# Kernel optimization log

Measured on AMD Instinct MI355X. Metric: run time of the kernel, lower is better.

Reference implementation:

```python
import jax, jax.numpy as jnp
import numpy as np

B, L = 8, 2048
AMP, ANG = 48, 16
H = 4
AQK, GQK = 12, 6   # amp/ang qk head dims
AV, GV = 12, 6     # amp/ang v head dims
LOOKBACK = 100


def setup_inputs() -> dict:
    key = jax.random.key(0)
    ks = jax.random.split(key, 16)
    def w(k, i, o):
        # kaiming-uniform-ish scale; stored [in, out] so forward is x @ W
        bound = 1.0 / np.sqrt(i)
        return jax.random.uniform(k, (i, o), jnp.float32, -bound, bound)
    return dict(
        x_ang=jax.random.normal(ks[0], (B, L, 2 * ANG), jnp.float32),
        x_amp=jax.random.normal(ks[1], (B, L, AMP), jnp.float32),
        Wq_amp=w(ks[2], AMP, H * AQK),
        Wk_amp=w(ks[3], AMP, H * AQK),
        Wv_amp=w(ks[4], AMP, H * AV),
        Wq_ang_r=w(ks[5], ANG, H * GQK),
        Wq_ang_i=w(ks[6], ANG, H * GQK),
        Wk_ang_r=w(ks[7], ANG, H * GQK),
        Wk_ang_i=w(ks[8], ANG, H * GQK),
        Wv_ang_r=w(ks[9], ANG, H * GV),
        Wv_ang_i=w(ks[10], ANG, H * GV),
        Wout_amp=w(ks[11], H * AV, AMP),
        bout_amp=jax.random.uniform(ks[12], (AMP,), jnp.float32, -0.1, 0.1),
        Wout_ang_r=w(ks[13], H * GV, ANG),
        Wout_ang_i=w(ks[14], H * GV, ANG),
    )


def _clin(xr, xi, Wr, Wi):
    # complex linear: (xr + i xi) @ (Wr + i Wi)
    return xr @ Wr - xi @ Wi, xr @ Wi + xi @ Wr


def reference(x_ang, x_amp, Wq_amp, Wk_amp, Wv_amp,
              Wq_ang_r, Wq_ang_i, Wk_ang_r, Wk_ang_i,
              Wv_ang_r, Wv_ang_i, Wout_amp, bout_amp,
              Wout_ang_r, Wout_ang_i):
    Bb, Ll, CA = x_ang.shape
    ang_r, ang_i = jnp.split(x_ang, 2, axis=-1)

    def heads(x, hd):  # [B,L,H*hd] -> [B,H,L,hd]
        return x.reshape(Bb, Ll, H, hd).transpose(0, 2, 1, 3)

    q_amp = heads(x_amp @ Wq_amp, AQK)
    k_amp = heads(x_amp @ Wk_amp, AQK)
    qar, qai = _clin(ang_r, ang_i, Wq_ang_r, Wq_ang_i)
    kar, kai = _clin(ang_r, ang_i, Wk_ang_r, Wk_ang_i)
    q = jnp.concatenate([heads(qar, GQK), heads(qai, GQK), q_amp], axis=-1)  # [B,H,L,24]
    k = jnp.concatenate([heads(kar, GQK), heads(kai, GQK), k_amp], axis=-1)

    v_amp = heads(x_amp @ Wv_amp, AV)
    var, vai = _clin(ang_r, ang_i, Wv_ang_r, Wv_ang_i)
    v = jnp.concatenate([heads(var, GV), heads(vai, GV), v_amp], axis=-1)  # [B,H,L,24]

    scale = 1.0 / jnp.sqrt(jnp.asarray(q.shape[-1], q.dtype))
    scores = jnp.einsum('bhqd,bhkd->bhqk', q, k) * scale
    idx = jnp.arange(Ll)
    valid = (idx[None, :] <= idx[:, None]) & (idx[None, :] >= idx[:, None] - (LOOKBACK - 1))
    mask = jnp.where(valid, jnp.asarray(0.0, scores.dtype), jnp.finfo(scores.dtype).min)
    attn = jax.nn.softmax(scores + mask, axis=-1)
    out = jnp.einsum('bhqk,bhkd->bhqd', attn, v)  # [B,H,L,24]

    o_ang_r, o_ang_i, o_amp = jnp.split(out, [GV, 2 * GV], axis=-1)

    def merge(x):  # [B,H,L,hd] -> [B,L,H*hd]
        return x.transpose(0, 2, 1, 3).reshape(Bb, Ll, -1)

    out_amp = merge(o_amp) @ Wout_amp + bout_amp
    out_ang_r, out_ang_i = _clin(merge(o_ang_r), merge(o_ang_i), Wout_ang_r, Wout_ang_i)
    return (out_ang_r, out_ang_i, out_amp)
```

## Files before the change

### kernel.cpp

```cpp
#include <hip/hip_runtime.h>
#include <hip/hip_bf16.h>
#include <hip/hip_fp16.h>

constexpr int B = 8;
constexpr int L = 2048;
constexpr int ANG = 16;
constexpr int AMP = 48;
constexpr int H = 4;
constexpr int AQK = 12, GQK = 6;
constexpr int AV = 12, GV = 6;
constexpr int HD = 2 * GQK + AQK;
constexpr int LOOKBACK = 100;
constexpr int NTOK = B * L;

typedef __fp16 f16x2 __attribute__((ext_vector_type(2)));

__device__ inline f16x2 pkrtz(float a, float b) {
    return __builtin_amdgcn_cvt_pkrtz(a, b);
}
__device__ inline float2 up2(f16x2 v) { return make_float2((float)v[0], (float)v[1]); }

union F4H { float4 v; f16x2 h[4]; };

constexpr int TQ     = 64;
constexpr int GROUPS = 4;
constexpr int CHUNK  = 25;
constexpr int MAXK   = TQ + LOOKBACK - 1;
constexpr int NT     = L / TQ;

struct StageT { f16x2 xall[MAXK][41]; };
struct TileT  {
    float4 Ks[MAXK][3];
    float4 Vs[MAXK][3];
    float4 Qs[TQ][7];
};
union SharedU { StageT s; TileT t; };

__device__ inline void proj_row(const f16x2* __restrict__ xrow, int h,
                                const float* __restrict__ Wamp,
                                const float* __restrict__ Wang_r,
                                const float* __restrict__ Wang_i,
                                float out[24])
{
    float a[12];
    #pragma unroll
    for (int c = 0; c < 12; ++c) a[c] = 0.f;
    #pragma unroll
    for (int i2 = 0; i2 < 24; ++i2) {
        float2 x2 = up2(xrow[i2]);
        const float* w0 = Wamp + (2 * i2) * 48 + h * AQK;
        const float* w1 = Wamp + (2 * i2 + 1) * 48 + h * AQK;
        #pragma unroll
        for (int c = 0; c < 12; ++c)
            a[c] += x2.x * w0[c] + x2.y * w1[c];
    }
    float rr[6], im[6];
    #pragma unroll
    for (int c = 0; c < 6; ++c) { rr[c] = 0.f; im[c] = 0.f; }
    #pragma unroll
    for (int i2 = 0; i2 < 8; ++i2) {
        float2 xr2 = up2(xrow[24 + i2]);
        float2 xi2 = up2(xrow[32 + i2]);
        const float* wr0 = Wang_r + (2 * i2) * 24 + h * GQK;
        const float* wi0 = Wang_i + (2 * i2) * 24 + h * GQK;
        const float* wr1 = Wang_r + (2 * i2 + 1) * 24 + h * GQK;
        const float* wi1 = Wang_i + (2 * i2 + 1) * 24 + h * GQK;
        #pragma unroll
        for (int c = 0; c < 6; ++c) {
            rr[c] += xr2.x * wr0[c] - xi2.x * wi0[c] + xr2.y * wr1[c] - xi2.y * wi1[c];
            im[c] += xr2.x * wi0[c] + xi2.x * wr0[c] + xr2.y * wi1[c] + xi2.y * wr1[c];
        }
    }
    #pragma unroll
    for (int c = 0; c < 6; ++c) { out[c] = rr[c]; out[6 + c] = im[c]; }
    #pragma unroll
    for (int c = 0; c < 12; ++c) out[12 + c] = a[c];
}

__global__ __launch_bounds__(256, 2) void fused_qkv_attn5_kernel(
    const float* __restrict__ x_ang, const float* __restrict__ x_amp,
    const float* __restrict__ Wq_amp, const float* __restrict__ Wk_amp,
    const float* __restrict__ Wv_amp,
    const float* __restrict__ Wq_ang_r, const float* __restrict__ Wq_ang_i,
    const float* __restrict__ Wk_ang_r, const float* __restrict__ Wk_ang_i,
    const float* __restrict__ Wv_ang_r, const float* __restrict__ Wv_ang_i,
    float* __restrict__ att)
{
    __shared__ SharedU u;

    const int tid = threadIdx.x;
    const int bh  = blockIdx.x / NT;
    const int qt  = blockIdx.x % NT;
    const int b   = bh / H, h = bh % H;
    const int q0  = qt * TQ;
    int kmin = q0 - (LOOKBACK - 1); if (kmin < 0) kmin = 0;
    const int nrows = q0 + TQ - kmin;
    const int qoff  = q0 - kmin;

    {
        const float4* xm4 = (const float4*)(x_amp + ((size_t)b * L + kmin) * AMP);
        const float4* xg4 = (const float4*)(x_ang + ((size_t)b * L + kmin) * (2 * ANG));
        int namp = nrows * 12;
        int ntot = namp + nrows * 8;
        for (int c = tid; c < ntot; c += 256) {
            if (c < namp) {
                int r = c / 12, i = c % 12;
                float4 t4 = xm4[c];
                u.s.xall[r][2 * i]     = pkrtz(t4.x, t4.y);
                u.s.xall[r][2 * i + 1] = pkrtz(t4.z, t4.w);
            } else {
                int c2 = c - namp;
                int r = c2 / 8, i = c2 % 8;
                float4 t4 = xg4[c2];
                u.s.xall[r][24 + 2 * i]     = pkrtz(t4.x, t4.y);
                u.s.xall[r][24 + 2 * i + 1] = pkrtz(t4.z, t4.w);
            }
        }
    }
    __syncthreads();

    const bool kvact = (tid < nrows);
    const bool qact  = (tid >= 192);
    const int  qrow  = tid - 192;

    float kd[24], vd[24], qd[24];
    if (kvact) {
        const f16x2* xrow = u.s.xall[tid];
        proj_row(xrow, h, Wk_amp, Wk_ang_r, Wk_ang_i, kd);
        proj_row(xrow, h, Wv_amp, Wv_ang_r, Wv_ang_i, vd);
    }
    if (qact) {
        const f16x2* xrow = u.s.xall[qoff + qrow];
        proj_row(xrow, h, Wq_amp, Wq_ang_r, Wq_ang_i, qd);
    }
    __syncthreads();

    if (kvact) {
        int r = tid;
        #pragma unroll
        for (int sl = 0; sl < 3; ++sl) {
            F4H pk_, pv_;
            #pragma unroll
            for (int j = 0; j < 4; ++j) {
                pk_.h[j] = pkrtz(kd[8 * sl + 2 * j], kd[8 * sl + 2 * j + 1]);
                pv_.h[j] = pkrtz(vd[8 * sl + 2 * j], vd[8 * sl + 2 * j + 1]);
            }
            u.t.Ks[r][sl] = pk_.v;
            u.t.Vs[r][sl] = pv_.v;
        }
    } else if (tid < MAXK) {
        float4 z = make_float4(0.f, 0.f, 0.f, 0.f);
        #pragma unroll
        for (int sl = 0; sl < 3; ++sl) { u.t.Ks[tid][sl] = z; u.t.Vs[tid][sl] = z; }
    }
    if (qact) {
        #pragma unroll
        for (int s = 0; s < 6; ++s)
            u.t.Qs[qrow][s] = make_float4(qd[4*s], qd[4*s+1], qd[4*s+2], qd[4*s+3]);
    }
    __syncthreads();

    const int lane = tid & 63;
    const int w    = tid >> 6;
    const int q16  = lane & 15;
    const int g    = lane >> 4;
    const int ql   = w * 16 + q16;
    const int qi   = q0 + ql;

    float qf[24];
    #pragma unroll
    for (int s = 0; s < 6; ++s) {
        float4 t4 = u.t.Qs[ql][s];
        qf[4*s] = t4.x; qf[4*s+1] = t4.y; qf[4*s+2] = t4.z; qf[4*s+3] = t4.w;
    }

    const float scale = 0.2041241452319315f;
    int j0 = qi - (LOOKBACK - 1); if (j0 < 0) j0 = 0;
    const int jstart = j0 + g;

    float sc[CHUNK];
    #pragma unroll
    for (int t = 0; t < CHUNK; ++t) {
        int j = jstart + t * GROUPS;
        int r = j - kmin;
        F4H k0, k1, k2;
        k0.v = u.t.Ks[r][0]; k1.v = u.t.Ks[r][1]; k2.v = u.t.Ks[r][2];
        float d = 0.f;
        #pragma unroll
        for (int jj = 0; jj < 4; ++jj) {
            float2 a0 = up2(k0.h[jj]); d += a0.x * qf[2*jj]      + a0.y * qf[2*jj+1];
            float2 a1 = up2(k1.h[jj]); d += a1.x * qf[8 + 2*jj]  + a1.y * qf[8 + 2*jj+1];
            float2 a2 = up2(k2.h[jj]); d += a2.x * qf[16 + 2*jj] + a2.y * qf[16 + 2*jj+1];
        }
        sc[t] = (j <= qi) ? d * scale : -3.0e38f;
    }
    float m = sc[0];
    #pragma unroll
    for (int t = 1; t < CHUNK; ++t) m = fmaxf(m, sc[t]);
    float ssum = 0.f;
    #pragma unroll
    for (int t = 0; t < CHUNK; ++t) {
        float p = __expf(sc[t] - m);
        p = (sc[t] > -1.0e37f) ? p : 0.f;
        sc[t] = p;
        ssum += p;
    }
    float o[24];
    #pragma unroll
    for (int e = 0; e < 24; ++e) o[e] = 0.f;
    #pragma unroll
    for (int t = 0; t < CHUNK; ++t) {
        float p = sc[t];
        int j = jstart + t * GROUPS;
        int r = j - kmin;
        F4H v0, v1, v2;
        v0.v = u.t.Vs[r][0]; v1.v = u.t.Vs[r][1]; v2.v = u.t.Vs[r][2];
        #pragma unroll
        for (int jj = 0; jj < 4; ++jj) {
            float2 a0 = up2(v0.h[jj]); o[2*jj]      += p * a0.x; o[2*jj+1]      += p * a0.y;
            float2 a1 = up2(v1.h[jj]); o[8 + 2*jj]  += p * a1.x; o[8 + 2*jj+1]  += p * a1.y;
            float2 a2 = up2(v2.h[jj]); o[16 + 2*jj] += p * a2.x; o[16 + 2*jj+1] += p * a2.y;
        }
    }

    #pragma unroll
    for (int d = 16; d <= 32; d <<= 1) {
        float m2 = __shfl_xor(m, d);
        float s2 = __shfl_xor(ssum, d);
        float mm = fmaxf(m, m2);
        float c1 = __expf(m - mm);
        float c2 = __expf(m2 - mm);
        ssum = ssum * c1 + s2 * c2;
        #pragma unroll
        for (int e = 0; e < 24; ++e)
            o[e] = o[e] * c1 + __shfl_xor(o[e], d) * c2;
        m = mm;
    }
    float inv = 1.f / ssum;

    {
        float4* dst = (float4*)att + (size_t)(b * L + qi) * 24 + h * 6;
        if (g == 0) {
            dst[0] = make_float4(o[0]*inv,  o[1]*inv,  o[2]*inv,  o[3]*inv);
            dst[4] = make_float4(o[16]*inv, o[17]*inv, o[18]*inv, o[19]*inv);
        } else if (g == 1) {
            dst[1] = make_float4(o[4]*inv,  o[5]*inv,  o[6]*inv,  o[7]*inv);
            dst[5] = make_float4(o[20]*inv, o[21]*inv, o[22]*inv, o[23]*inv);
        } else if (g == 2) {
            dst[2] = make_float4(o[8]*inv,  o[9]*inv,  o[10]*inv, o[11]*inv);
        } else {
            dst[3] = make_float4(o[12]*inv, o[13]*inv, o[14]*inv, o[15]*inv);
        }
    }
}

constexpr int PJ_AMP_BLOCKS = (NTOK * 12) / 256;
constexpr int PJ_ANG_BLOCKS = (NTOK * 4) / 256;

__global__ __launch_bounds__(256) void proj4_kernel(
    const float* __restrict__ att,
    const float* __restrict__ Wout_amp, const float* __restrict__ bout_amp,
    const float* __restrict__ Wout_ang_r, const float* __restrict__ Wout_ang_i,
    float* __restrict__ out)
{
    constexpr size_t ANG_OUT = (size_t)NTOK * ANG;
    int bid = blockIdx.x;

    if (bid < PJ_AMP_BLOCKS) {
        int gidx = bid * 256 + threadIdx.x;
        int c4   = (gidx % 12) * 4;
        int tok  = gidx / 12;
        const float4* at4 = (const float4*)att + (size_t)tok * 24;

        float a[48];
        #pragma unroll
        for (int h = 0; h < H; ++h) {
            #pragma unroll
            for (int i = 0; i < 3; ++i) {
                float4 t = at4[h * 6 + 3 + i];
                a[h*12 + 4*i+0]=t.x; a[h*12 + 4*i+1]=t.y;
                a[h*12 + 4*i+2]=t.z; a[h*12 + 4*i+3]=t.w;
            }
        }
        float4 acc = *(const float4*)(bout_amp + c4);
        #pragma unroll
        for (int i = 0; i < 48; ++i) {
            float4 w = *(const float4*)(Wout_amp + i * 48 + c4);
            acc.x += a[i]*w.x; acc.y += a[i]*w.y; acc.z += a[i]*w.z; acc.w += a[i]*w.w;
        }
        *(float4*)(out + 2*ANG_OUT + (size_t)tok * 48 + c4) = acc;
    } else {
        int gidx = (bid - PJ_AMP_BLOCKS) * 256 + threadIdx.x;
        int c4   = (gidx % 4) * 4;
        int tok  = gidx / 4;
        const float4* at4 = (const float4*)att + (size_t)tok * 24;

        float ar[24], ai[24];
        #pragma unroll
        for (int h = 0; h < H; ++h) {
            float4 t0 = at4[h*6+0], t1 = at4[h*6+1], t2 = at4[h*6+2];
            ar[h*6+0]=t0.x; ar[h*6+1]=t0.y; ar[h*6+2]=t0.z; ar[h*6+3]=t0.w;
            ar[h*6+4]=t1.x; ar[h*6+5]=t1.y;
            ai[h*6+0]=t1.z; ai[h*6+1]=t1.w;
            ai[h*6+2]=t2.x; ai[h*6+3]=t2.y; ai[h*6+4]=t2.z; ai[h*6+5]=t2.w;
        }
        float4 accr = make_float4(0.f,0.f,0.f,0.f);
        float4 acci = make_float4(0.f,0.f,0.f,0.f);
        #pragma unroll
        for (int i = 0; i < 24; ++i) {
            float4 wr = *(const float4*)(Wout_ang_r + i * 16 + c4);
            float4 wi = *(const float4*)(Wout_ang_i + i * 16 + c4);
            float r = ar[i], im = ai[i];
            accr.x += r*wr.x - im*wi.x;  accr.y += r*wr.y - im*wi.y;
            accr.z += r*wr.z - im*wi.z;  accr.w += r*wr.w - im*wi.w;
            acci.x += r*wi.x + im*wr.x;  acci.y += r*wi.y + im*wr.y;
            acci.z += r*wi.z + im*wr.z;  acci.w += r*wi.w + im*wr.w;
        }
        *(float4*)(out + (size_t)tok * 16 + c4)           = accr;
        *(float4*)(out + ANG_OUT + (size_t)tok * 16 + c4) = acci;
    }
}

extern "C" void kernel_launch(void* const* d_in, const int* in_sizes, int n_in,
                              void* d_out, int out_size, void* d_ws, size_t ws_size,
                              hipStream_t stream)
{
    const float* x_ang      = (const float*)d_in[0];
    const float* x_amp      = (const float*)d_in[1];
    const float* Wq_amp     = (const float*)d_in[2];
    const float* Wk_amp     = (const float*)d_in[3];
    const float* Wv_amp     = (const float*)d_in[4];
    const float* Wq_ang_r   = (const float*)d_in[5];
    const float* Wq_ang_i   = (const float*)d_in[6];
    const float* Wk_ang_r   = (const float*)d_in[7];
    const float* Wk_ang_i   = (const float*)d_in[8];
    const float* Wv_ang_r   = (const float*)d_in[9];
    const float* Wv_ang_i   = (const float*)d_in[10];
    const float* Wout_amp   = (const float*)d_in[11];
    const float* bout_amp   = (const float*)d_in[12];
    const float* Wout_ang_r = (const float*)d_in[13];
    const float* Wout_ang_i = (const float*)d_in[14];

    float* out = (float*)d_out;
    float* att = (float*)d_ws;

    fused_qkv_attn5_kernel<<<B * H * NT, 256, 0, stream>>>(
        x_ang, x_amp, Wq_amp, Wk_amp, Wv_amp,
        Wq_ang_r, Wq_ang_i, Wk_ang_r, Wk_ang_i, Wv_ang_r, Wv_ang_i,
        att);

    proj4_kernel<<<PJ_AMP_BLOCKS + PJ_ANG_BLOCKS, 256, 0, stream>>>(
        att, Wout_amp, bout_amp, Wout_ang_r, Wout_ang_i, out);
}
```

Measured before the change: 152.6 us.

## Split QKV projection into separate kernel and use fdot2 for QK scores

Unfuses the QKV projection from the attention kernel. A new kernel projects each token exactly once into fp16 Q/K/V buffers in workspace, and the attention kernel loads K/V tiles and Q rows from global memory. This removes the redundant K/V projection of the lookback halo rows (about 163 rows per 64-query tile) and the idle lanes during projection. The cost is an extra kernel launch and a global-memory round trip for Q/K/V. The QK dot product now uses packed fp16 fdot2 instructions, with the query also rounded to fp16.

```diff
diff --git a/kernel.cpp b/kernel.cpp
--- a/kernel.cpp
+++ b/kernel.cpp
@@ -1,5 +1,4 @@
 #include <hip/hip_runtime.h>
-#include <hip/hip_bf16.h>
 #include <hip/hip_fp16.h>
 
 constexpr int B = 8;
@@ -8,8 +7,6 @@
 constexpr int AMP = 48;
 constexpr int H = 4;
 constexpr int AQK = 12, GQK = 6;
-constexpr int AV = 12, GV = 6;
-constexpr int HD = 2 * GQK + AQK;
 constexpr int LOOKBACK = 100;
 constexpr int NTOK = B * L;
 
@@ -20,73 +17,120 @@
 }
 __device__ inline float2 up2(f16x2 v) { return make_float2((float)v[0], (float)v[1]); }
 
+__device__ inline float fdot2f(f16x2 a, f16x2 b, float c) {
+#if __has_builtin(__builtin_amdgcn_fdot2)
+    return __builtin_amdgcn_fdot2(a, b, c, false);
+#else
+    return c + (float)a[0] * (float)b[0] + (float)a[1] * (float)b[1];
+#endif
+}
+
 union F4H { float4 v; f16x2 h[4]; };
 
-constexpr int TQ     = 64;
-constexpr int GROUPS = 4;
-constexpr int CHUNK  = 25;
-constexpr int MAXK   = TQ + LOOKBACK - 1;
-constexpr int NT     = L / TQ;
-
-struct StageT { f16x2 xall[MAXK][41]; };
-struct TileT  {
-    float4 Ks[MAXK][3];
-    float4 Vs[MAXK][3];
-    float4 Qs[TQ][7];
-};
-union SharedU { StageT s; TileT t; };
-
-__device__ inline void proj_row(const f16x2* __restrict__ xrow, int h,
-                                const float* __restrict__ Wamp,
-                                const float* __restrict__ Wang_r,
-                                const float* __restrict__ Wang_i,
-                                float out[24])
-{
-    float a[12];
-    #pragma unroll
-    for (int c = 0; c < 12; ++c) a[c] = 0.f;
-    #pragma unroll
-    for (int i2 = 0; i2 < 24; ++i2) {
-        float2 x2 = up2(xrow[i2]);
-        const float* w0 = Wamp + (2 * i2) * 48 + h * AQK;
-        const float* w1 = Wamp + (2 * i2 + 1) * 48 + h * AQK;
-        #pragma unroll
-        for (int c = 0; c < 12; ++c)
-            a[c] += x2.x * w0[c] + x2.y * w1[c];
-    }
-    float rr[6], im[6];
-    #pragma unroll
-    for (int c = 0; c < 6; ++c) { rr[c] = 0.f; im[c] = 0.f; }
-    #pragma unroll
-    for (int i2 = 0; i2 < 8; ++i2) {
-        float2 xr2 = up2(xrow[24 + i2]);
-        float2 xi2 = up2(xrow[32 + i2]);
-        const float* wr0 = Wang_r + (2 * i2) * 24 + h * GQK;
-        const float* wi0 = Wang_i + (2 * i2) * 24 + h * GQK;
-        const float* wr1 = Wang_r + (2 * i2 + 1) * 24 + h * GQK;
-        const float* wi1 = Wang_i + (2 * i2 + 1) * 24 + h * GQK;
-        #pragma unroll
-        for (int c = 0; c < 6; ++c) {
-            rr[c] += xr2.x * wr0[c] - xi2.x * wi0[c] + xr2.y * wr1[c] - xi2.y * wi1[c];
-            im[c] += xr2.x * wi0[c] + xi2.x * wr0[c] + xr2.y * wi1[c] + xi2.y * wr1[c];
-        }
-    }
-    #pragma unroll
-    for (int c = 0; c < 6; ++c) { out[c] = rr[c]; out[6 + c] = im[c]; }
-    #pragma unroll
-    for (int c = 0; c < 12; ++c) out[12 + c] = a[c];
-}
-
-__global__ __launch_bounds__(256, 2) void fused_qkv_attn5_kernel(
+constexpr int QT = 64;
+constexpr int QKV_BLOCKS = NTOK / QT;
+
+__global__ __launch_bounds__(256) void qkv6_kernel(
     const float* __restrict__ x_ang, const float* __restrict__ x_amp,
     const float* __restrict__ Wq_amp, const float* __restrict__ Wk_amp,
     const float* __restrict__ Wv_amp,
     const float* __restrict__ Wq_ang_r, const float* __restrict__ Wq_ang_i,
     const float* __restrict__ Wk_ang_r, const float* __restrict__ Wk_ang_i,
     const float* __restrict__ Wv_ang_r, const float* __restrict__ Wv_ang_i,
-    float* __restrict__ att)
+    __fp16* __restrict__ qg, __fp16* __restrict__ kg, __fp16* __restrict__ vg)
 {
-    __shared__ SharedU u;
+    __shared__ float xs[QT][81];
+    const int tid  = threadIdx.x;
+    const int tok0 = blockIdx.x * QT;
+
+    {
+        const float4* xm4 = (const float4*)(x_amp + (size_t)tok0 * AMP);
+        for (int c = tid; c < QT * 12; c += 256) {
+            int r = c / 12, i = c % 12;
+            float4 t = xm4[c];
+            float* p = &xs[r][4 * i];
+            p[0]=t.x; p[1]=t.y; p[2]=t.z; p[3]=t.w;
+        }
+        const float4* xg4 = (const float4*)(x_ang + (size_t)tok0 * (2 * ANG));
+        for (int c = tid; c < QT * 8; c += 256) {
+            int r = c / 8, i = c % 8;
+            float4 t = xg4[c];
+            float* p = &xs[r][48 + 4 * i];
+            p[0]=t.x; p[1]=t.y; p[2]=t.z; p[3]=t.w;
+        }
+    }
+    __syncthreads();
+
+    const int h  = tid >> 6;
+    const int tl = tid & 63;
+
+    float qd[24], kd[24], vd[24];
+    #pragma unroll
+    for (int c = 0; c < 24; ++c) { qd[c]=0.f; kd[c]=0.f; vd[c]=0.f; }
+
+    #pragma unroll
+    for (int i = 0; i < AMP; ++i) {
+        float x = xs[tl][i];
+        const float* wq = Wq_amp + i * 48 + h * AQK;
+        const float* wk = Wk_amp + i * 48 + h * AQK;
+        const float* wv = Wv_amp + i * 48 + h * AQK;
+        #pragma unroll
+        for (int c = 0; c < 12; ++c) {
+            qd[12+c] += x * wq[c];
+            kd[12+c] += x * wk[c];
+            vd[12+c] += x * wv[c];
+        }
+    }
+    #pragma unroll
+    for (int i = 0; i < ANG; ++i) {
+        float xr = xs[tl][48 + i], xi = xs[tl][64 + i];
+        const float* wqr = Wq_ang_r + i * 24 + h * GQK;
+        const float* wqi = Wq_ang_i + i * 24 + h * GQK;
+        const float* wkr = Wk_ang_r + i * 24 + h * GQK;
+        const float* wki = Wk_ang_i + i * 24 + h * GQK;
+        const float* wvr = Wv_ang_r + i * 24 + h * GQK;
+        const float* wvi = Wv_ang_i + i * 24 + h * GQK;
+        #pragma unroll
+        for (int c = 0; c < 6; ++c) {
+            qd[c]   += xr * wqr[c] - xi * wqi[c];
+            qd[6+c] += xr * wqi[c] + xi * wqr[c];
+            kd[c]   += xr * wkr[c] - xi * wki[c];
+            kd[6+c] += xr * wki[c] + xi * wkr[c];
+            vd[c]   += xr * wvr[c] - xi * wvi[c];
+            vd[6+c] += xr * wvi[c] + xi * wvr[c];
+        }
+    }
+
+    const int bb = tok0 / L;
+    const int ll = (tok0 % L) + tl;
+    const size_t row = ((size_t)(bb * H + h) * L + ll) * 3;
+    #pragma unroll
+    for (int sl = 0; sl < 3; ++sl) {
+        F4H fq, fk, fv;
+        #pragma unroll
+        for (int j = 0; j < 4; ++j) {
+            fq.h[j] = pkrtz(qd[8*sl + 2*j], qd[8*sl + 2*j + 1]);
+            fk.h[j] = pkrtz(kd[8*sl + 2*j], kd[8*sl + 2*j + 1]);
+            fv.h[j] = pkrtz(vd[8*sl + 2*j], vd[8*sl + 2*j + 1]);
+        }
+        ((float4*)qg)[row + sl] = fq.v;
+        ((float4*)kg)[row + sl] = fk.v;
+        ((float4*)vg)[row + sl] = fv.v;
+    }
+}
+
+constexpr int TQ     = 64;
+constexpr int GROUPS = 4;
+constexpr int CHUNK  = 25;
+constexpr int MAXK   = TQ + LOOKBACK - 1;
+constexpr int NT     = L / TQ;
+
+__global__ __launch_bounds__(256, 2) void attn7_kernel(
+    const __fp16* __restrict__ qg, const __fp16* __restrict__ kg,
+    const __fp16* __restrict__ vg, float* __restrict__ att)
+{
+    __shared__ float4 Ks[MAXK][3];
+    __shared__ float4 Vs[MAXK][3];
 
     const int tid = threadIdx.x;
     const int bh  = blockIdx.x / NT;
@@ -95,68 +139,20 @@
     const int q0  = qt * TQ;
     int kmin = q0 - (LOOKBACK - 1); if (kmin < 0) kmin = 0;
     const int nrows = q0 + TQ - kmin;
-    const int qoff  = q0 - kmin;
 
     {
-        const float4* xm4 = (const float4*)(x_amp + ((size_t)b * L + kmin) * AMP);
-        const float4* xg4 = (const float4*)(x_ang + ((size_t)b * L + kmin) * (2 * ANG));
-        int namp = nrows * 12;
-        int ntot = namp + nrows * 8;
+        const float4* kb = (const float4*)kg + ((size_t)bh * L + kmin) * 3;
+        const float4* vb = (const float4*)vg + ((size_t)bh * L + kmin) * 3;
+        int ntot = nrows * 3;
         for (int c = tid; c < ntot; c += 256) {
-            if (c < namp) {
-                int r = c / 12, i = c % 12;
-                float4 t4 = xm4[c];
-                u.s.xall[r][2 * i]     = pkrtz(t4.x, t4.y);
-                u.s.xall[r][2 * i + 1] = pkrtz(t4.z, t4.w);
-            } else {
-                int c2 = c - namp;
-                int r = c2 / 8, i = c2 % 8;
-                float4 t4 = xg4[c2];
-                u.s.xall[r][24 + 2 * i]     = pkrtz(t4.x, t4.y);
-                u.s.xall[r][24 + 2 * i + 1] = pkrtz(t4.z, t4.w);
-            }
-        }
-    }
-    __syncthreads();
-
-    const bool kvact = (tid < nrows);
-    const bool qact  = (tid >= 192);
-    const int  qrow  = tid - 192;
-
-    float kd[24], vd[24], qd[24];
-    if (kvact) {
-        const f16x2* xrow = u.s.xall[tid];
-        proj_row(xrow, h, Wk_amp, Wk_ang_r, Wk_ang_i, kd);
-        proj_row(xrow, h, Wv_amp, Wv_ang_r, Wv_ang_i, vd);
-    }
-    if (qact) {
-        const f16x2* xrow = u.s.xall[qoff + qrow];
-        proj_row(xrow, h, Wq_amp, Wq_ang_r, Wq_ang_i, qd);
-    }
-    __syncthreads();
-
-    if (kvact) {
-        int r = tid;
-        #pragma unroll
-        for (int sl = 0; sl < 3; ++sl) {
-            F4H pk_, pv_;
-            #pragma unroll
-            for (int j = 0; j < 4; ++j) {
-                pk_.h[j] = pkrtz(kd[8 * sl + 2 * j], kd[8 * sl + 2 * j + 1]);
-                pv_.h[j] = pkrtz(vd[8 * sl + 2 * j], vd[8 * sl + 2 * j + 1]);
-            }
-            u.t.Ks[r][sl] = pk_.v;
-            u.t.Vs[r][sl] = pv_.v;
-        }
-    } else if (tid < MAXK) {
+            Ks[c / 3][c % 3] = kb[c];
+            Vs[c / 3][c % 3] = vb[c];
+        }
         float4 z = make_float4(0.f, 0.f, 0.f, 0.f);
-        #pragma unroll
-        for (int sl = 0; sl < 3; ++sl) { u.t.Ks[tid][sl] = z; u.t.Vs[tid][sl] = z; }
-    }
-    if (qact) {
-        #pragma unroll
-        for (int s = 0; s < 6; ++s)
-            u.t.Qs[qrow][s] = make_float4(qd[4*s], qd[4*s+1], qd[4*s+2], qd[4*s+3]);
+        for (int c = ntot + tid; c < MAXK * 3; c += 256) {
+            Ks[c / 3][c % 3] = z;
+            Vs[c / 3][c % 3] = z;
+        }
     }
     __syncthreads();
 
@@ -167,11 +163,15 @@
     const int ql   = w * 16 + q16;
     const int qi   = q0 + ql;
 
-    float qf[24];
-    #pragma unroll
-    for (int s = 0; s < 6; ++s) {
-        float4 t4 = u.t.Qs[ql][s];
-        qf[4*s] = t4.x; qf[4*s+1] = t4.y; qf[4*s+2] = t4.z; qf[4*s+3] = t4.w;
+    f16x2 qh[12];
+    {
+        const float4* qrow = (const float4*)qg + ((size_t)bh * L + qi) * 3;
+        F4H a0, a1, a2;
+        a0.v = qrow[0]; a1.v = qrow[1]; a2.v = qrow[2];
+        #pragma unroll
+        for (int j = 0; j < 4; ++j) {
+            qh[j] = a0.h[j]; qh[4 + j] = a1.h[j]; qh[8 + j] = a2.h[j];
+        }
     }
 
     const float scale = 0.2041241452319315f;
@@ -184,14 +184,14 @@
         int j = jstart + t * GROUPS;
         int r = j - kmin;
         F4H k0, k1, k2;
-        k0.v = u.t.Ks[r][0]; k1.v = u.t.Ks[r][1]; k2.v = u.t.Ks[r][2];
+        k0.v = Ks[r][0]; k1.v = Ks[r][1]; k2.v = Ks[r][2];
         float d = 0.f;
         #pragma unroll
-        for (int jj = 0; jj < 4; ++jj) {
-            float2 a0 = up2(k0.h[jj]); d += a0.x * qf[2*jj]      + a0.y * qf[2*jj+1];
-            float2 a1 = up2(k1.h[jj]); d += a1.x * qf[8 + 2*jj]  + a1.y * qf[8 + 2*jj+1];
-            float2 a2 = up2(k2.h[jj]); d += a2.x * qf[16 + 2*jj] + a2.y * qf[16 + 2*jj+1];
-        }
+        for (int jj = 0; jj < 4; ++jj) d = fdot2f(qh[jj],     k0.h[jj], d);
+        #pragma unroll
+        for (int jj = 0; jj < 4; ++jj) d = fdot2f(qh[4 + jj], k1.h[jj], d);
+        #pragma unroll
+        for (int jj = 0; jj < 4; ++jj) d = fdot2f(qh[8 + jj], k2.h[jj], d);
         sc[t] = (j <= qi) ? d * scale : -3.0e38f;
     }
     float m = sc[0];
@@ -213,13 +213,15 @@
         float p = sc[t];
         int j = jstart + t * GROUPS;
         int r = j - kmin;
-        F4H v0, v1, v2;
-        v0.v = u.t.Vs[r][0]; v1.v = u.t.Vs[r][1]; v2.v = u.t.Vs[r][2];
-        #pragma unroll
-        for (int jj = 0; jj < 4; ++jj) {
-            float2 a0 = up2(v0.h[jj]); o[2*jj]      += p * a0.x; o[2*jj+1]      += p * a0.y;
-            float2 a1 = up2(v1.h[jj]); o[8 + 2*jj]  += p * a1.x; o[8 + 2*jj+1]  += p * a1.y;
-            float2 a2 = up2(v2.h[jj]); o[16 + 2*jj] += p * a2.x; o[16 + 2*jj+1] += p * a2.y;
+        #pragma unroll
+        for (int sl = 0; sl < 3; ++sl) {
+            F4H vv; vv.v = Vs[r][sl];
+            #pragma unroll
+            for (int jj = 0; jj < 4; ++jj) {
+                float2 a = up2(vv.h[jj]);
+                o[8*sl + 2*jj]     += p * a.x;
+                o[8*sl + 2*jj + 1] += p * a.y;
+            }
         }
     }
 
@@ -342,12 +344,19 @@
     const float* Wout_ang_i = (const float*)d_in[14];
 
     float* out = (float*)d_out;
-    float* att = (float*)d_ws;
-
-    fused_qkv_attn5_kernel<<<B * H * NT, 256, 0, stream>>>(
+
+    const size_t NQKV = (size_t)NTOK * H * 24;
+    __fp16* qg = (__fp16*)d_ws;
+    __fp16* kg = qg + NQKV;
+    __fp16* vg = kg + NQKV;
+    float*  att = (float*)(vg + NQKV);
+
+    qkv6_kernel<<<QKV_BLOCKS, 256, 0, stream>>>(
         x_ang, x_amp, Wq_amp, Wk_amp, Wv_amp,
         Wq_ang_r, Wq_ang_i, Wk_ang_r, Wk_ang_i, Wv_ang_r, Wv_ang_i,
-        att);
+        qg, kg, vg);
+
+    attn7_kernel<<<B * H * NT, 256, 0, stream>>>(qg, kg, vg, att);
 
     proj4_kernel<<<PJ_AMP_BLOCKS + PJ_ANG_BLOCKS, 256, 0, stream>>>(
         att, Wout_amp, bout_amp, Wout_ang_r, Wout_ang_i, out);
```

New measurement: 140.5 us. 7.9% less time.
